# Kernel optimization log

Hardware: AMD Instinct MI355X
Metric: run time of the kernel (lower is better)

The kernel has to match this reference:

```python
import jax, jax.numpy as jnp
import numpy as np

EMBED = 1024; HEADS = 16; HEAD_DIM = 64; NB = 12; SEQ = 256; GRID = 16; HID = 2816
RMS_EPS = 1e-5; LN_EPS = 1e-6; ROPE_BASE = 10000.0; CLS = 1


def _freqs_cis_2d(grid, n_elem, base=ROPE_BASE, cls_token_num=CLS):
    half = n_elem // 2
    fr = 1.0 / (base ** (jnp.arange(0, half, 2)[: half // 2].astype(jnp.float32) / half))
    t = jnp.arange(grid, dtype=jnp.float32)
    f = t[:, None] * fr[None, :]  # (grid, n_elem//4)
    fg = jnp.concatenate([
        jnp.broadcast_to(f[:, None, :], (grid, grid, f.shape[1])),
        jnp.broadcast_to(f[None, :, :], (grid, grid, f.shape[1])),
    ], -1)  # (grid, grid, half)
    cache = jnp.stack([jnp.cos(fg), jnp.sin(fg)], -1).reshape(grid * grid, half, 2)
    return jnp.concatenate([jnp.zeros((cls_token_num, half, 2), cache.dtype), cache], 0)


def _rope(x, fc):
    # x: (B,S,H,hd); fc: (S, hd//2, 2)
    xr = x.astype(jnp.float32).reshape(x.shape[:-1] + (-1, 2))
    cos = fc[None, :, None, :, 0]; sin = fc[None, :, None, :, 1]
    out = jnp.stack([xr[..., 0] * cos - xr[..., 1] * sin,
                     xr[..., 1] * cos + xr[..., 0] * sin], -1)
    return out.reshape(x.shape).astype(x.dtype)


def _rmsnorm(x, w):
    xf = x.astype(jnp.float32)
    return (xf * jax.lax.rsqrt(jnp.mean(xf * xf, -1, keepdims=True) + RMS_EPS)).astype(x.dtype) * w


def _layernorm(x, g, b):
    m = jnp.mean(x, -1, keepdims=True)
    v = jnp.var(x, -1, keepdims=True)
    return (x - m) * jax.lax.rsqrt(v + LN_EPS) * g + b


def _block(h, p, fc, mask_bias):
    wqkv, wo, w1, w2, w3, anw, fnw = p
    B, S, D = h.shape
    a = _rmsnorm(h, anw)
    qkv = a @ wqkv  # (B,S,3D)
    q, k, v = jnp.split(qkv, [D, 2 * D], -1)
    q = _rope(q.reshape(B, S, HEADS, HEAD_DIM), fc)
    k = _rope(k.reshape(B, S, HEADS, HEAD_DIM), fc)
    v = v.reshape(B, S, HEADS, HEAD_DIM)
    scale = 1.0 / np.sqrt(HEAD_DIM).astype(np.float32)
    scores = jnp.einsum('bqhd,bkhd->bhqk', q.astype(jnp.float32), k.astype(jnp.float32)) * scale
    attn = jax.nn.softmax(scores + mask_bias, axis=-1)
    o = jnp.einsum('bhqk,bkhd->bqhd', attn, v.astype(jnp.float32)).reshape(B, S, D).astype(h.dtype)
    h = h + o @ wo
    f = _rmsnorm(h, fnw)
    h = h + (jax.nn.silu(f @ w1) * (f @ w3)) @ w2
    return h


def setup_inputs() -> dict:
    key = jax.random.key(0)
    ks = jax.random.split(key, 12)
    s = 0.02
    return {
        'x': jax.random.normal(ks[0], (32, SEQ, 3 * 16 * 16), jnp.float32),
        'cond': jax.random.normal(ks[1], (32, 1024), jnp.float32),
        'patch_w': jax.random.normal(ks[2], (768, EMBED), jnp.float32) * s,
        'patch_b': jnp.zeros((EMBED,), jnp.float32),
        'ln_g': jnp.ones((EMBED,), jnp.float32),
        'ln_b': jnp.zeros((EMBED,), jnp.float32),
        'pos_embed': jax.random.normal(ks[3], (1, SEQ + 1, EMBED), jnp.float32) * s,
        'cond_w': jax.random.normal(ks[4], (1024, EMBED), jnp.float32) * s,
        'cond_b': jnp.zeros((EMBED,), jnp.float32),
        'wqkv': jax.random.normal(ks[5], (NB, EMBED, 3 * EMBED), jnp.float32) * s,
        'wo': jax.random.normal(ks[6], (NB, EMBED, EMBED), jnp.float32) * s,
        'w1': jax.random.normal(ks[7], (NB, EMBED, HID), jnp.float32) * s,
        'w2': jax.random.normal(ks[8], (NB, HID, EMBED), jnp.float32) * s,
        'w3': jax.random.normal(ks[9], (NB, EMBED, HID), jnp.float32) * s,
        'attn_norm_w': jnp.ones((NB, EMBED), jnp.float32),
        'ffn_norm_w': jnp.ones((NB, EMBED), jnp.float32),
    }


def reference(x, cond, patch_w, patch_b, ln_g, ln_b, pos_embed, cond_w, cond_b,
              wqkv, wo, w1, w2, w3, attn_norm_w, ffn_norm_w):
    h = x @ patch_w + patch_b                       # (B, SEQ, D)
    c = cond @ cond_w + cond_b                      # (B, D)
    h = jnp.concatenate([c[:, None, :], h], 1) + pos_embed  # (B, SEQ+1, D)
    h = _layernorm(h, ln_g, ln_b)
    S = h.shape[1]
    fc = _freqs_cis_2d(GRID, HEAD_DIM)[:S]
    mask_bias = jnp.where(jnp.tril(jnp.ones((S, S), bool)), 0.0, -jnp.inf)[None, None]
    def step(carry, p):
        return _block(carry, p, fc, mask_bias), None
    h, _ = jax.lax.scan(step, h, (wqkv, wo, w1, w2, w3, attn_norm_w, ffn_norm_w))
    return h
```

## Files before the change

kernel.cpp:

```cpp
#include <hip/hip_runtime.h>
#include <hip/hip_bf16.h>
#include <cstdint>
#include <cstddef>

#define NBLK   12
#define EMBED  1024
#define SEQT   257
#define BATCH  32
#define NHEADS 16
#define HD     64
#define HIDF   2816
#define MV     (BATCH*SEQT)
#define MPAD   8320
#define SP     288

typedef __attribute__((ext_vector_type(8))) short short8;
typedef __attribute__((ext_vector_type(4))) float f32x4;

__device__ __forceinline__ short f2bs(float f) {
  unsigned u = __float_as_uint(f);
  unsigned r = (u + 0x7fffu + ((u >> 16) & 1u)) >> 16;
  return (short)r;
}
__device__ __forceinline__ float bs2f(short s) {
  return __uint_as_float(((unsigned)(unsigned short)s) << 16);
}

__device__ __forceinline__ void async_copy16(void* lds, const void* g) {
  __builtin_amdgcn_global_load_lds(
      (const __attribute__((address_space(1))) unsigned int*)g,
      (__attribute__((address_space(3))) unsigned int*)lds,
      16, 0, 0);
}

template<int MODE>
__global__ __launch_bounds__(256, 2)
void gemm_bt(const short* __restrict__ A, const short* __restrict__ B,
             void* __restrict__ Out, const float* __restrict__ Resid,
             const short* __restrict__ Aux,
             int M, int N, int K, int Mvalid)
{
  __shared__ short sA[128 * 64];
  __shared__ short sB[128 * 64];
  const int tid  = threadIdx.x;
  const int wid  = tid >> 6;
  const int lane = tid & 63;
  const int r16  = lane & 15;
  const int quad = lane >> 4;
  const int m0 = blockIdx.y * 128;
  const int n0 = blockIdx.x * 128;
  const int wm = (wid >> 1) * 64;
  const int wn = (wid & 1) * 64;

  f32x4 acc[4][4];
#pragma unroll
  for (int i = 0; i < 4; ++i)
#pragma unroll
    for (int j = 0; j < 4; ++j)
      acc[i][j] = (f32x4){0.f, 0.f, 0.f, 0.f};

  const int nk = K >> 6;
  for (int kt = 0; kt < nk; ++kt) {
    const int k0 = kt << 6;
    __syncthreads();
#pragma unroll
    for (int i = 0; i < 4; ++i) {
      const int c   = wid * 256 + i * 64;
      const int cl  = c + lane;
      const int row = cl >> 3;
      const int col = (cl & 7) << 3;
      async_copy16(&sA[c * 8], A + (size_t)(m0 + row) * K + k0 + col);
      async_copy16(&sB[c * 8], B + (size_t)(n0 + row) * K + k0 + col);
    }
    asm volatile("s_waitcnt vmcnt(0)" ::: "memory");
    __syncthreads();
#pragma unroll
    for (int ks = 0; ks < 2; ++ks) {
      short8 af[4], bf[4];
#pragma unroll
      for (int t = 0; t < 4; ++t) {
        af[t] = *(const short8*)&sA[(wm + t * 16 + r16) * 64 + ks * 32 + quad * 8];
        bf[t] = *(const short8*)&sB[(wn + t * 16 + r16) * 64 + ks * 32 + quad * 8];
      }
#pragma unroll
      for (int i = 0; i < 4; ++i)
#pragma unroll
        for (int j = 0; j < 4; ++j)
          acc[i][j] = __builtin_amdgcn_mfma_f32_16x16x32_bf16(af[i], bf[j], acc[i][j], 0, 0, 0);
    }
  }

#pragma unroll
  for (int i = 0; i < 4; ++i) {
#pragma unroll
    for (int r = 0; r < 4; ++r) {
      const int row = m0 + wm + i * 16 + quad * 4 + r;
      if (row >= Mvalid) continue;
#pragma unroll
      for (int j = 0; j < 4; ++j) {
        const int col = n0 + wn + j * 16 + r16;
        const size_t idx = (size_t)row * N + col;
        const float v = acc[i][j][r];
        if (MODE == 0) {
          ((short*)Out)[idx] = f2bs(v);
        } else if (MODE == 1) {
          ((float*)Out)[idx] = v;
        } else if (MODE == 2) {
          ((float*)Out)[idx] = v + Resid[idx];
        } else {
          const float u3 = bs2f(Aux[idx]);
          const float sig = 1.f / (1.f + __expf(-v));
          ((short*)Out)[idx] = f2bs(v * sig * u3);
        }
      }
    }
  }
}

__global__ void transpose_cast(const float* __restrict__ src, short* __restrict__ dst,
                               int K, int N)
{
  __shared__ float t[32][33];
  const int n0 = blockIdx.x * 32;
  const int k0 = blockIdx.y * 32;
  const int tx = threadIdx.x;
  const int ty = threadIdx.y;
#pragma unroll
  for (int i = 0; i < 32; i += 8)
    t[ty + i][tx] = src[(size_t)(k0 + ty + i) * N + n0 + tx];
  __syncthreads();
#pragma unroll
  for (int i = 0; i < 32; i += 8)
    dst[(size_t)(n0 + ty + i) * K + k0 + tx] = f2bs(t[tx][ty + i]);
}

__global__ void cast_bf16(const float* __restrict__ src, short* __restrict__ dst, int n)
{
  const int i = blockIdx.x * 256 + threadIdx.x;
  if (i < n) dst[i] = f2bs(src[i]);
}

__global__ void freqs_k(float* __restrict__ fc)
{
  const int idx = blockIdx.x * 256 + threadIdx.x;
  if (idx >= SEQT * 32) return;
  const int s = idx >> 5;
  const int j = idx & 31;
  float c = 0.f, sn = 0.f;
  if (s != 0) {
    const int p = s - 1;
    const int pos = (j < 16) ? (p >> 4) : (p & 15);
    const int fi = (j < 16) ? j : (j - 16);
    const float fr = __powf(10000.f, -(float)fi / 16.f);
    const float ang = (float)pos * fr;
    c = cosf(ang); sn = sinf(ang);
  }
  fc[idx * 2]     = c;
  fc[idx * 2 + 1] = sn;
}

__global__ void cond_embed_k(const float* __restrict__ cond, const float* __restrict__ w,
                             const float* __restrict__ bias, float* __restrict__ out)
{
  const int b = blockIdx.y;
  const int o = blockIdx.x * 256 + threadIdx.x;
  const float* cr = cond + (size_t)b * EMBED;
  float acc = 0.f;
  for (int in = 0; in < 1024; ++in)
    acc += cr[in] * w[(size_t)in * EMBED + o];
  out[(size_t)b * EMBED + o] = acc + bias[o];
}

__global__ void assemble_ln_k(const float* __restrict__ tmp, const float* __restrict__ cemb,
                              const float* __restrict__ pb, const float* __restrict__ pos,
                              const float* __restrict__ g, const float* __restrict__ beta,
                              float* __restrict__ h)
{
  const int r = blockIdx.x;
  const int bb = r / SEQT;
  const int s = r % SEQT;
  const int t = threadIdx.x;
  float4 v;
  if (s == 0) {
    v = ((const float4*)(cemb + (size_t)bb * EMBED))[t];
  } else {
    v = ((const float4*)(tmp + (size_t)(bb * 256 + s - 1) * EMBED))[t];
    const float4 pb4 = ((const float4*)pb)[t];
    v.x += pb4.x; v.y += pb4.y; v.z += pb4.z; v.w += pb4.w;
  }
  const float4 p4 = ((const float4*)(pos + (size_t)s * EMBED))[t];
  v.x += p4.x; v.y += p4.y; v.z += p4.z; v.w += p4.w;

  float s1 = v.x + v.y + v.z + v.w;
  float s2 = v.x * v.x + v.y * v.y + v.z * v.z + v.w * v.w;
  __shared__ float sb[8];
  const int lane = t & 63, wid = t >> 6;
#pragma unroll
  for (int off = 32; off > 0; off >>= 1) {
    s1 += __shfl_down(s1, off, 64);
    s2 += __shfl_down(s2, off, 64);
  }
  if (lane == 0) { sb[wid] = s1; sb[4 + wid] = s2; }
  __syncthreads();
  const float tot   = sb[0] + sb[1] + sb[2] + sb[3];
  const float totsq = sb[4] + sb[5] + sb[6] + sb[7];
  const float mean = tot * (1.f / 1024.f);
  const float var  = totsq * (1.f / 1024.f) - mean * mean;
  const float sc = rsqrtf(var + 1e-6f);
  const float4 g4 = ((const float4*)g)[t];
  const float4 be4 = ((const float4*)beta)[t];
  float4 o;
  o.x = (v.x - mean) * sc * g4.x + be4.x;
  o.y = (v.y - mean) * sc * g4.y + be4.y;
  o.z = (v.z - mean) * sc * g4.z + be4.z;
  o.w = (v.w - mean) * sc * g4.w + be4.w;
  ((float4*)(h + (size_t)r * EMBED))[t] = o;
}

__global__ void rmsnorm_k(const float* __restrict__ h, const float* __restrict__ w,
                          short* __restrict__ out)
{
  const int r = blockIdx.x;
  const int t = threadIdx.x;
  const float4 v = ((const float4*)(h + (size_t)r * EMBED))[t];
  float ss = v.x * v.x + v.y * v.y + v.z * v.z + v.w * v.w;
  __shared__ float sb[4];
  const int lane = t & 63, wid = t >> 6;
#pragma unroll
  for (int off = 32; off > 0; off >>= 1) ss += __shfl_down(ss, off, 64);
  if (lane == 0) sb[wid] = ss;
  __syncthreads();
  const float tot = sb[0] + sb[1] + sb[2] + sb[3];
  const float sc = rsqrtf(tot * (1.f / 1024.f) + 1e-5f);
  const float4 w4 = ((const float4*)w)[t];
  short* op = out + (size_t)r * EMBED + t * 4;
  op[0] = f2bs(v.x * sc * w4.x);
  op[1] = f2bs(v.y * sc * w4.y);
  op[2] = f2bs(v.z * sc * w4.z);
  op[3] = f2bs(v.w * sc * w4.w);
}

__global__ void rope_k(const short* __restrict__ qkv, const float* __restrict__ fc,
                       short* __restrict__ Q, short* __restrict__ Kt, short* __restrict__ Vt)
{
  const int r = blockIdx.x;
  const int bb = r / SEQT;
  const int s = r % SEQT;
  const int t = threadIdx.x;
  const short* row = qkv + (size_t)r * 3072;
#pragma unroll
  for (int ii = 0; ii < 2; ++ii) {
    const int i = t + ii * 256;
    const int hh = i >> 5;
    const int j = i & 31;
    const float cs = fc[(s * 32 + j) * 2];
    const float sn = fc[(s * 32 + j) * 2 + 1];
    const size_t ob = (((size_t)bb * NHEADS + hh) * SP + s) * HD + 2 * j;
    {
      const float x0 = bs2f(row[hh * HD + 2 * j]);
      const float x1 = bs2f(row[hh * HD + 2 * j + 1]);
      Q[ob]     = f2bs(x0 * cs - x1 * sn);
      Q[ob + 1] = f2bs(x1 * cs + x0 * sn);
    }
    {
      const float x0 = bs2f(row[EMBED + hh * HD + 2 * j]);
      const float x1 = bs2f(row[EMBED + hh * HD + 2 * j + 1]);
      Kt[ob]     = f2bs(x0 * cs - x1 * sn);
      Kt[ob + 1] = f2bs(x1 * cs + x0 * sn);
    }
  }
#pragma unroll
  for (int ii = 0; ii < 4; ++ii) {
    const int i = t + ii * 256;
    const int hh = i >> 6;
    const int d = i & 63;
    Vt[(((size_t)bb * NHEADS + hh) * HD + d) * SP + s] = row[2048 + i];
  }
}

__global__ __launch_bounds__(64)
void attn_k(const short* __restrict__ Q, const short* __restrict__ Kt,
            const short* __restrict__ Vt, short* __restrict__ O)
{
  const int qt = blockIdx.x;
  const int hh = blockIdx.y;
  const int bb = blockIdx.z;
  const int lane = threadIdx.x;
  const int r16 = lane & 15;
  const int quad = lane >> 4;

  const size_t bh = (size_t)bb * NHEADS + hh;
  const short* qbase = Q  + bh * SP * HD;
  const short* kbase = Kt + bh * SP * HD;
  const short* vbase = Vt + bh * HD * SP;

  const int qrow_l = qt * 16 + r16;
  const short8 qf0 = *(const short8*)(qbase + qrow_l * HD + quad * 8);
  const short8 qf1 = *(const short8*)(qbase + qrow_l * HD + 32 + quad * 8);

  float m_i[4], l_i[4];
  f32x4 oacc[4];
#pragma unroll
  for (int r = 0; r < 4; ++r) { m_i[r] = -INFINITY; l_i[r] = 0.f; }
#pragma unroll
  for (int t = 0; t < 4; ++t) oacc[t] = (f32x4){0.f, 0.f, 0.f, 0.f};

  __shared__ float pls[16][33];

  const int nkb = qt / 2 + 1;
  for (int kbi = 0; kbi < nkb; ++kbi) {
    const int key0 = kbi * 32 + r16;
    const int key1 = key0 + 16;
    const short8 kf00 = *(const short8*)(kbase + key0 * HD + quad * 8);
    const short8 kf01 = *(const short8*)(kbase + key0 * HD + 32 + quad * 8);
    const short8 kf10 = *(const short8*)(kbase + key1 * HD + quad * 8);
    const short8 kf11 = *(const short8*)(kbase + key1 * HD + 32 + quad * 8);

    f32x4 s0 = (f32x4){0.f, 0.f, 0.f, 0.f};
    f32x4 s1 = (f32x4){0.f, 0.f, 0.f, 0.f};
    s0 = __builtin_amdgcn_mfma_f32_16x16x32_bf16(qf0, kf00, s0, 0, 0, 0);
    s0 = __builtin_amdgcn_mfma_f32_16x16x32_bf16(qf1, kf01, s0, 0, 0, 0);
    s1 = __builtin_amdgcn_mfma_f32_16x16x32_bf16(qf0, kf10, s1, 0, 0, 0);
    s1 = __builtin_amdgcn_mfma_f32_16x16x32_bf16(qf1, kf11, s1, 0, 0, 0);

    const int col0 = kbi * 32 + r16;
    const int col1 = col0 + 16;
    float p0[4], p1[4];
#pragma unroll
    for (int r = 0; r < 4; ++r) {
      const int qrow = qt * 16 + quad * 4 + r;
      float v0 = (col0 <= qrow) ? s0[r] * 0.125f : -INFINITY;
      float v1 = (col1 <= qrow) ? s1[r] * 0.125f : -INFINITY;
      float mx = fmaxf(v0, v1);
#pragma unroll
      for (int off = 1; off < 16; off <<= 1)
        mx = fmaxf(mx, __shfl_xor(mx, off, 64));
      const float mnew = fmaxf(m_i[r], mx);
      const float alpha = __expf(m_i[r] - mnew);
      m_i[r] = mnew;
      p0[r] = __expf(v0 - mnew);
      p1[r] = __expf(v1 - mnew);
      float rs = p0[r] + p1[r];
#pragma unroll
      for (int off = 1; off < 16; off <<= 1)
        rs += __shfl_xor(rs, off, 64);
      l_i[r] = l_i[r] * alpha + rs;
#pragma unroll
      for (int t = 0; t < 4; ++t) oacc[t][r] *= alpha;
    }

    __syncthreads();
#pragma unroll
    for (int r = 0; r < 4; ++r) {
      pls[quad * 4 + r][r16]      = p0[r];
      pls[quad * 4 + r][16 + r16] = p1[r];
    }
    __syncthreads();
    short8 pf;
#pragma unroll
    for (int j = 0; j < 8; ++j) pf[j] = f2bs(pls[r16][quad * 8 + j]);

#pragma unroll
    for (int t = 0; t < 4; ++t) {
      const short8 vf = *(const short8*)(vbase + (t * 16 + r16) * SP + kbi * 32 + quad * 8);
      oacc[t] = __builtin_amdgcn_mfma_f32_16x16x32_bf16(pf, vf, oacc[t], 0, 0, 0);
    }
  }

#pragma unroll
  for (int r = 0; r < 4; ++r) {
    const int qrow = qt * 16 + quad * 4 + r;
    if (qrow >= SEQT) continue;
    const float inv = 1.f / l_i[r];
#pragma unroll
    for (int t = 0; t < 4; ++t)
      O[((size_t)(bb * SEQT + qrow)) * EMBED + hh * HD + t * 16 + r16] = f2bs(oacc[t][r] * inv);
  }
}

extern "C" void kernel_launch(void* const* d_in, const int* in_sizes, int n_in,
                              void* d_out, int out_size, void* d_ws, size_t ws_size,
                              hipStream_t stream)
{
  (void)in_sizes; (void)n_in; (void)out_size; (void)ws_size;
  const float* x      = (const float*)d_in[0];
  const float* cond   = (const float*)d_in[1];
  const float* patchW = (const float*)d_in[2];
  const float* patchB = (const float*)d_in[3];
  const float* lnG    = (const float*)d_in[4];
  const float* lnB    = (const float*)d_in[5];
  const float* posE   = (const float*)d_in[6];
  const float* condW  = (const float*)d_in[7];
  const float* condB  = (const float*)d_in[8];
  const float* wqkv   = (const float*)d_in[9];
  const float* wo     = (const float*)d_in[10];
  const float* w1     = (const float*)d_in[11];
  const float* w2     = (const float*)d_in[12];
  const float* w3     = (const float*)d_in[13];
  const float* anw    = (const float*)d_in[14];
  const float* fnw    = (const float*)d_in[15];

  char* p = (char*)d_ws;
  auto alloc = [&](size_t bytes) -> void* {
    void* r = (void*)p;
    p += (bytes + 255) & ~(size_t)255;
    return r;
  };

  short* wqkvT = (short*)alloc((size_t)NBLK * 3072 * 1024 * 2);
  short* woT   = (short*)alloc((size_t)NBLK * 1024 * 1024 * 2);
  short* w1T   = (short*)alloc((size_t)NBLK * HIDF * 1024 * 2);
  short* w2T   = (short*)alloc((size_t)NBLK * 1024 * HIDF * 2);
  short* w3T   = (short*)alloc((size_t)NBLK * HIDF * 1024 * 2);
  short* pwT   = (short*)alloc((size_t)1024 * 768 * 2);
  short* xb    = (short*)alloc((size_t)8192 * 768 * 2);
  float* tmp   = (float*)alloc((size_t)8192 * 1024 * 4);
  float* cemb  = (float*)alloc((size_t)32 * 1024 * 4);
  float* hbuf  = (float*)alloc((size_t)MPAD * 1024 * 4);
  short* abuf  = (short*)alloc((size_t)MPAD * 1024 * 2);
  short* qkvb  = (short*)alloc((size_t)MPAD * 3072 * 2);
  short* qb    = (short*)alloc((size_t)BATCH * NHEADS * SP * HD * 2);
  short* kbuf  = (short*)alloc((size_t)BATCH * NHEADS * SP * HD * 2);
  short* vtb   = (short*)alloc((size_t)BATCH * NHEADS * HD * SP * 2);
  short* ob    = (short*)alloc((size_t)MPAD * 1024 * 2);
  short* u3b   = (short*)alloc((size_t)MPAD * HIDF * 2);
  short* gbuf  = (short*)alloc((size_t)MPAD * HIDF * 2);
  float* fc    = (float*)alloc((size_t)SEQT * 32 * 2 * 4);

  const dim3 tb32(32, 8);
  for (int l = 0; l < NBLK; ++l) {
    transpose_cast<<<dim3(3072 / 32, 1024 / 32), tb32, 0, stream>>>(
        wqkv + (size_t)l * 1024 * 3072, wqkvT + (size_t)l * 3072 * 1024, 1024, 3072);
    transpose_cast<<<dim3(1024 / 32, 1024 / 32), tb32, 0, stream>>>(
        wo + (size_t)l * 1024 * 1024, woT + (size_t)l * 1024 * 1024, 1024, 1024);
    transpose_cast<<<dim3(HIDF / 32, 1024 / 32), tb32, 0, stream>>>(
        w1 + (size_t)l * 1024 * HIDF, w1T + (size_t)l * HIDF * 1024, 1024, HIDF);
    transpose_cast<<<dim3(1024 / 32, HIDF / 32), tb32, 0, stream>>>(
        w2 + (size_t)l * HIDF * 1024, w2T + (size_t)l * 1024 * HIDF, HIDF, 1024);
    transpose_cast<<<dim3(HIDF / 32, 1024 / 32), tb32, 0, stream>>>(
        w3 + (size_t)l * 1024 * HIDF, w3T + (size_t)l * HIDF * 1024, 1024, HIDF);
  }
  transpose_cast<<<dim3(1024 / 32, 768 / 32), tb32, 0, stream>>>(patchW, pwT, 768, 1024);
  cast_bf16<<<(8192 * 768 + 255) / 256, 256, 0, stream>>>(x, xb, 8192 * 768);
  freqs_k<<<(SEQT * 32 + 255) / 256, 256, 0, stream>>>(fc);
  cond_embed_k<<<dim3(4, 32), 256, 0, stream>>>(cond, condW, condB, cemb);
  gemm_bt<1><<<dim3(1024 / 128, 8192 / 128), 256, 0, stream>>>(
      xb, pwT, tmp, nullptr, nullptr, 8192, 1024, 768, 8192);
  assemble_ln_k<<<MV, 256, 0, stream>>>(tmp, cemb, patchB, posE, lnG, lnB, hbuf);

  for (int l = 0; l < NBLK; ++l) {
    rmsnorm_k<<<MV, 256, 0, stream>>>(hbuf, anw + l * 1024, abuf);
    gemm_bt<0><<<dim3(3072 / 128, MPAD / 128), 256, 0, stream>>>(
        abuf, wqkvT + (size_t)l * 3072 * 1024, qkvb, nullptr, nullptr, MPAD, 3072, 1024, MV);
    rope_k<<<MV, 256, 0, stream>>>(qkvb, fc, qb, kbuf, vtb);
    attn_k<<<dim3(17, NHEADS, BATCH), 64, 0, stream>>>(qb, kbuf, vtb, ob);
    gemm_bt<2><<<dim3(1024 / 128, MPAD / 128), 256, 0, stream>>>(
        ob, woT + (size_t)l * 1024 * 1024, hbuf, hbuf, nullptr, MPAD, 1024, 1024, MV);
    rmsnorm_k<<<MV, 256, 0, stream>>>(hbuf, fnw + l * 1024, abuf);
    gemm_bt<0><<<dim3(HIDF / 128, MPAD / 128), 256, 0, stream>>>(
        abuf, w3T + (size_t)l * HIDF * 1024, u3b, nullptr, nullptr, MPAD, HIDF, 1024, MV);
    gemm_bt<3><<<dim3(HIDF / 128, MPAD / 128), 256, 0, stream>>>(
        abuf, w1T + (size_t)l * HIDF * 1024, gbuf, nullptr, u3b, MPAD, HIDF, 1024, MV);
    float* outp = (l == NBLK - 1) ? (float*)d_out : hbuf;
    gemm_bt<2><<<dim3(1024 / 128, MPAD / 128), 256, 0, stream>>>(
        gbuf, w2T + (size_t)l * 1024 * HIDF, outp, hbuf, nullptr, MPAD, 1024, HIDF, MV);
  }
}
```

Baseline: 6.495 ms.

## Swizzle GEMM LDS layout, group tile order for L2 reuse, batch weight transposes

```diff
diff --git a/kernel.cpp b/kernel.cpp
--- a/kernel.cpp
+++ b/kernel.cpp
@@ -47,8 +47,19 @@
   const int lane = tid & 63;
   const int r16  = lane & 15;
   const int quad = lane >> 4;
-  const int m0 = blockIdx.y * 128;
-  const int n0 = blockIdx.x * 128;
+
+  const int nTn = gridDim.x, nTm = gridDim.y;
+  const int pid = blockIdx.y * nTn + blockIdx.x;
+  const int GROUP_M = 8;
+  const int group_size = GROUP_M * nTn;
+  const int group_id = pid / group_size;
+  const int first_m = group_id * GROUP_M;
+  const int gsz = min(GROUP_M, nTm - first_m);
+  const int pid_m = first_m + (pid % group_size) % gsz;
+  const int pid_n = (pid % group_size) / gsz;
+  const int m0 = pid_m * 128;
+  const int n0 = pid_n * 128;
+
   const int wm = (wid >> 1) * 64;
   const int wn = (wid & 1) * 64;
 
@@ -65,22 +76,24 @@
     __syncthreads();
 #pragma unroll
     for (int i = 0; i < 4; ++i) {
-      const int c   = wid * 256 + i * 64;
-      const int cl  = c + lane;
-      const int row = cl >> 3;
-      const int col = (cl & 7) << 3;
-      async_copy16(&sA[c * 8], A + (size_t)(m0 + row) * K + k0 + col);
-      async_copy16(&sB[c * 8], B + (size_t)(n0 + row) * K + k0 + col);
+      const int cbase = wid * 256 + i * 64;
+      const int s   = cbase + lane;
+      const int row = s >> 3;
+      const int cc  = (s & 7) ^ (row & 7);
+      async_copy16(&sA[cbase * 8], A + (size_t)(m0 + row) * K + k0 + cc * 8);
+      async_copy16(&sB[cbase * 8], B + (size_t)(n0 + row) * K + k0 + cc * 8);
     }
     asm volatile("s_waitcnt vmcnt(0)" ::: "memory");
     __syncthreads();
 #pragma unroll
     for (int ks = 0; ks < 2; ++ks) {
       short8 af[4], bf[4];
+      const int cbase_l = ks * 4 + quad;
+      const int cphys = cbase_l ^ (r16 & 7);
 #pragma unroll
       for (int t = 0; t < 4; ++t) {
-        af[t] = *(const short8*)&sA[(wm + t * 16 + r16) * 64 + ks * 32 + quad * 8];
-        bf[t] = *(const short8*)&sB[(wn + t * 16 + r16) * 64 + ks * 32 + quad * 8];
+        af[t] = *(const short8*)&sA[(wm + t * 16 + r16) * 64 + cphys * 8];
+        bf[t] = *(const short8*)&sB[(wn + t * 16 + r16) * 64 + cphys * 8];
       }
 #pragma unroll
       for (int i = 0; i < 4; ++i)
@@ -120,6 +133,8 @@
 __global__ void transpose_cast(const float* __restrict__ src, short* __restrict__ dst,
                                int K, int N)
 {
+  const size_t loff = (size_t)blockIdx.z * (size_t)K * N;
+  src += loff; dst += loff;
   __shared__ float t[32][33];
   const int n0 = blockIdx.x * 32;
   const int k0 = blockIdx.y * 32;
@@ -428,19 +443,12 @@
   float* fc    = (float*)alloc((size_t)SEQT * 32 * 2 * 4);
 
   const dim3 tb32(32, 8);
-  for (int l = 0; l < NBLK; ++l) {
-    transpose_cast<<<dim3(3072 / 32, 1024 / 32), tb32, 0, stream>>>(
-        wqkv + (size_t)l * 1024 * 3072, wqkvT + (size_t)l * 3072 * 1024, 1024, 3072);
-    transpose_cast<<<dim3(1024 / 32, 1024 / 32), tb32, 0, stream>>>(
-        wo + (size_t)l * 1024 * 1024, woT + (size_t)l * 1024 * 1024, 1024, 1024);
-    transpose_cast<<<dim3(HIDF / 32, 1024 / 32), tb32, 0, stream>>>(
-        w1 + (size_t)l * 1024 * HIDF, w1T + (size_t)l * HIDF * 1024, 1024, HIDF);
-    transpose_cast<<<dim3(1024 / 32, HIDF / 32), tb32, 0, stream>>>(
-        w2 + (size_t)l * HIDF * 1024, w2T + (size_t)l * 1024 * HIDF, HIDF, 1024);
-    transpose_cast<<<dim3(HIDF / 32, 1024 / 32), tb32, 0, stream>>>(
-        w3 + (size_t)l * 1024 * HIDF, w3T + (size_t)l * HIDF * 1024, 1024, HIDF);
-  }
-  transpose_cast<<<dim3(1024 / 32, 768 / 32), tb32, 0, stream>>>(patchW, pwT, 768, 1024);
+  transpose_cast<<<dim3(3072 / 32, 1024 / 32, NBLK), tb32, 0, stream>>>(wqkv, wqkvT, 1024, 3072);
+  transpose_cast<<<dim3(1024 / 32, 1024 / 32, NBLK), tb32, 0, stream>>>(wo, woT, 1024, 1024);
+  transpose_cast<<<dim3(HIDF / 32, 1024 / 32, NBLK), tb32, 0, stream>>>(w1, w1T, 1024, HIDF);
+  transpose_cast<<<dim3(1024 / 32, HIDF / 32, NBLK), tb32, 0, stream>>>(w2, w2T, HIDF, 1024);
+  transpose_cast<<<dim3(HIDF / 32, 1024 / 32, NBLK), tb32, 0, stream>>>(w3, w3T, 1024, HIDF);
+  transpose_cast<<<dim3(1024 / 32, 768 / 32, 1), tb32, 0, stream>>>(patchW, pwT, 768, 1024);
   cast_bf16<<<(8192 * 768 + 255) / 256, 256, 0, stream>>>(x, xb, 8192 * 768);
   freqs_k<<<(SEQT * 32 + 255) / 256, 256, 0, stream>>>(fc);
   cond_embed_k<<<dim3(4, 32), 256, 0, stream>>>(cond, condW, condB, cemb);
```

Result: faster. 5.836 ms (-10.1%).
